# Performance work log

Hardware: AMD Instinct MI355X
Metric: run time of the kernel (lower is better)

The kernel has to match this reference:

```python
import jax, jax.numpy as jnp
import numpy as np

H = 16
NUM_LANDMARKS = 32


def setup_inputs() -> dict:
    key = jax.random.key(0)
    ks = jax.random.split(key, 8)
    B, L, D, hd = 2, 2048, 1024, 64
    x = jax.random.normal(ks[0], (B, L, D), dtype=jnp.float32)
    wscale = 1.0 / np.sqrt(D)
    wq = jax.random.normal(ks[1], (D, D), dtype=jnp.float32) * wscale
    wk = jax.random.normal(ks[2], (D, D), dtype=jnp.float32) * wscale
    wv = jax.random.normal(ks[3], (D, D), dtype=jnp.float32) * wscale
    wo = jax.random.normal(ks[4], (D, D), dtype=jnp.float32) * wscale
    memory_gate = jnp.zeros((1,), dtype=jnp.float32)
    memory_decay = jnp.asarray(2.944, dtype=jnp.float32)
    # standard RoPE angle table: theta_j = 10000^(-2j/hd)
    inv_freq = 1.0 / (10000.0 ** (np.arange(0, hd, 2, dtype=np.float32) / hd))
    ang = np.outer(np.arange(L, dtype=np.float32), inv_freq)  # (L, hd//2)
    freqs_cos = jnp.asarray(np.cos(ang), dtype=jnp.float32)
    freqs_sin = jnp.asarray(np.sin(ang), dtype=jnp.float32)
    # previous-chunk memory: phi features are >= 0, Z accumulates ~NUM_LANDMARKS
    M_old = jax.random.normal(ks[5], (B, H, hd, hd), dtype=jnp.float32) * 0.1
    Z_old = jax.random.uniform(ks[6], (B, H, hd), dtype=jnp.float32) * NUM_LANDMARKS + 1.0
    return {"x": x, "wq": wq, "wk": wk, "wv": wv, "wo": wo,
            "memory_gate": memory_gate, "memory_decay": memory_decay,
            "freqs_cos": freqs_cos, "freqs_sin": freqs_sin,
            "M_old": M_old, "Z_old": Z_old}


def reference(x, wq, wk, wv, wo, memory_gate, memory_decay,
              freqs_cos, freqs_sin, M_old, Z_old):
    B, L, D = x.shape
    hd = D // H

    def proj(w):
        # nn.Linear: x @ W^T, then split heads -> (B, H, L, hd)
        return (x @ w.T).reshape(B, L, H, hd).transpose(0, 2, 1, 3)

    q_base, k_base, v = proj(wq), proj(wk), proj(wv)

    def rope(t):
        # complex multiply on adjacent pairs of the head dim
        tr = t.reshape(B, H, L, hd // 2, 2)
        t0, t1 = tr[..., 0], tr[..., 1]
        cos = freqs_cos[None, None]  # (1,1,L,hd//2)
        sin = freqs_sin[None, None]
        o0 = t0 * cos - t1 * sin
        o1 = t0 * sin + t1 * cos
        return jnp.stack([o0, o1], axis=-1).reshape(B, H, L, hd)

    q_rope, k_rope = rope(q_base), rope(k_base)

    # causal SDPA
    scale = 1.0 / jnp.sqrt(jnp.asarray(hd, dtype=q_rope.dtype))
    scores = jnp.einsum('bhqd,bhkd->bhqk', q_rope, k_rope) * scale
    causal = jnp.tril(jnp.ones((L, L), dtype=bool))
    scores = jnp.where(causal[None, None], scores, jnp.finfo(scores.dtype).min)
    attn = jax.nn.softmax(scores, axis=-1)
    local_out = jnp.einsum('bhqk,bhkd->bhqd', attn, v)

    # linear-attention memory read (uses un-rotated q_base)
    phi_Q = jax.nn.elu(q_base) + 1.0
    num = jnp.einsum('bhld,bhde->bhle', phi_Q, M_old)
    den = jnp.sum(phi_Q * Z_old[:, :, None, :], axis=-1, keepdims=True) + 1e-6
    global_out = num / den
    gate = jax.nn.sigmoid(memory_gate)  # (1,)
    out = local_out + gate * global_out

    # landmark compression: adaptive avg pool == uniform chunk means (L % M == 0)
    def landmarks(t):
        return t.reshape(B, H, NUM_LANDMARKS, L // NUM_LANDMARKS, hd).mean(axis=3)

    phi_K = jax.nn.elu(landmarks(k_base)) + 1.0
    landmark_v = landmarks(v)
    delta_M = jnp.einsum('bhmd,bhme->bhde', phi_K, landmark_v)
    delta_Z = phi_K.sum(axis=-2)

    decay = jax.nn.sigmoid(memory_decay)
    M_new = M_old * decay + delta_M
    Z_new = Z_old * decay + delta_Z

    out = out.transpose(0, 2, 1, 3).reshape(B, L, D)
    y = out @ wo.T
    return y, M_new, Z_new
```

## Files before the change

kernel.cpp:

```cpp
#include <hip/hip_runtime.h>
#include <math.h>

#define NH 16
#define HD 64
#define NB 2
#define LSEQ 2048
#define DM 1024
#define NLM 32

#define OUT_M 4194304
#define OUT_Z 4325376

typedef unsigned short u16;
typedef short bf16x8 __attribute__((ext_vector_type(8)));
typedef float f32x16 __attribute__((ext_vector_type(16)));
typedef unsigned short u16x4 __attribute__((ext_vector_type(4)));
typedef unsigned long long ull;

__device__ __forceinline__ float sigmoidf_(float x) { return 1.0f / (1.0f + __expf(-x)); }
__device__ __forceinline__ float phif_(float x) { return x > 0.0f ? x + 1.0f : __expf(x); }

__device__ __forceinline__ u16 f2b(float f) {
    union { float f; unsigned u; } v; v.f = f;
    unsigned r = v.u + 0x7FFFu + ((v.u >> 16) & 1u);
    return (u16)(r >> 16);
}
__device__ __forceinline__ float b2f(u16 b) {
    union { unsigned u; float f; } v; v.u = ((unsigned)b) << 16; return v.f;
}
__device__ __forceinline__ ull pack4(float a, float b, float c, float d) {
    return (ull)f2b(a) | ((ull)f2b(b) << 16) | ((ull)f2b(c) << 32) | ((ull)f2b(d) << 48);
}
__device__ __forceinline__ int cvtpkbf(float lo, float hi2) {
    int r;
    asm("v_cvt_pk_bf16_f32 %0, %1, %2" : "=v"(r) : "v"(lo), "v"(hi2));
    return r;
}
__device__ __forceinline__ void gload16(const u16* g, u16* l) {
    __builtin_amdgcn_global_load_lds(
        (const __attribute__((address_space(1))) void*)g,
        (__attribute__((address_space(3))) void*)l, 16, 0, 0);
}
__device__ __forceinline__ void block_sync_lds() {
    __builtin_amdgcn_sched_barrier(0);
    asm volatile("s_waitcnt lgkmcnt(0)" ::: "memory");
    __builtin_amdgcn_s_barrier();
    __builtin_amdgcn_sched_barrier(0);
}

__global__ __launch_bounds__(256) void cvt_all(
    const float* __restrict__ x, const float* __restrict__ wq,
    const float* __restrict__ wk, const float* __restrict__ wv,
    const float* __restrict__ wo, u16* __restrict__ dst) {
    size_t i = ((size_t)blockIdx.x * 256 + threadIdx.x) * 8;
    const float* src;
    size_t off;
    if (i < 4194304)      { src = x;  off = i; }
    else if (i < 5242880) { src = wq; off = i - 4194304; }
    else if (i < 6291456) { src = wk; off = i - 5242880; }
    else if (i < 7340032) { src = wv; off = i - 6291456; }
    else                  { src = wo; off = i - 7340032; }
    float4 a = *(const float4*)(src + off);
    float4 b = *(const float4*)(src + off + 4);
    u16 o[8] = {f2b(a.x), f2b(a.y), f2b(a.z), f2b(a.w),
                f2b(b.x), f2b(b.y), f2b(b.z), f2b(b.w)};
    *(int4*)(dst + i) = *(int4*)o;
}

template <int MODE>
__global__ __launch_bounds__(256) void gemm_mfma(
    const u16* __restrict__ A, const u16* __restrict__ W,
    float* __restrict__ Cf, u16* __restrict__ qb, u16* __restrict__ qrp,
    u16* __restrict__ kbp, u16* __restrict__ krp, u16* __restrict__ vbp,
    const float* __restrict__ fcos, const float* __restrict__ fsin) {
    __shared__ u16 As[128 * 64];
    __shared__ u16 Ws[128 * 64];
    const int tid = threadIdx.x;
    const int m0 = blockIdx.x * 128;
    const int n0 = blockIdx.y * 128;
    const int w = tid >> 6;
    const int lane = tid & 63;
    const int l31 = lane & 31;
    const int khalf = lane >> 5;
    const int wr0 = (w >> 1) * 64;
    const int wc0 = (w & 1) * 64;

    const u16* Ag = A + (size_t)m0 * DM;
    const u16* Wg = W + (size_t)n0 * DM;

    const int st_uoff[4] = {w * 4096, w * 4096 + 1024, w * 4096 + 2048, w * 4096 + 3072};
    int st_row[4], st_cc[4];
#pragma unroll
    for (int i = 0; i < 4; ++i) {
        const int off = st_uoff[i] + lane * 16;
        st_row[i] = off >> 7;
        st_cc[i] = ((off >> 4) & 7) ^ (st_row[i] & 7);
    }

    f32x16 acc[2][2];
#pragma unroll
    for (int mf = 0; mf < 2; ++mf)
#pragma unroll
        for (int nf = 0; nf < 2; ++nf)
#pragma unroll
            for (int i = 0; i < 16; ++i) acc[mf][nf][i] = 0.f;

    for (int k0 = 0; k0 < DM; k0 += 64) {
        __syncthreads();
#pragma unroll
        for (int i = 0; i < 4; ++i)
            gload16(Ag + (size_t)st_row[i] * DM + k0 + st_cc[i] * 8,
                    (u16*)((char*)As + st_uoff[i]));
#pragma unroll
        for (int i = 0; i < 4; ++i)
            gload16(Wg + (size_t)st_row[i] * DM + k0 + st_cc[i] * 8,
                    (u16*)((char*)Ws + st_uoff[i]));
        __syncthreads();
#pragma unroll
        for (int ko = 0; ko < 4; ++ko) {
            const int cl = ko * 2 + khalf;
            const int ra0 = wr0 + l31, ra1 = wr0 + 32 + l31;
            const int rb0 = wc0 + l31, rb1 = wc0 + 32 + l31;
            bf16x8 af0 = *(const bf16x8*)((char*)As + ra0 * 128 + ((cl ^ (ra0 & 7)) * 16));
            bf16x8 af1 = *(const bf16x8*)((char*)As + ra1 * 128 + ((cl ^ (ra1 & 7)) * 16));
            bf16x8 bf0 = *(const bf16x8*)((char*)Ws + rb0 * 128 + ((cl ^ (rb0 & 7)) * 16));
            bf16x8 bf1 = *(const bf16x8*)((char*)Ws + rb1 * 128 + ((cl ^ (rb1 & 7)) * 16));
            acc[0][0] = __builtin_amdgcn_mfma_f32_32x32x16_bf16(af0, bf0, acc[0][0], 0, 0, 0);
            acc[0][1] = __builtin_amdgcn_mfma_f32_32x32x16_bf16(af0, bf1, acc[0][1], 0, 0, 0);
            acc[1][0] = __builtin_amdgcn_mfma_f32_32x32x16_bf16(af1, bf0, acc[1][0], 0, 0, 0);
            acc[1][1] = __builtin_amdgcn_mfma_f32_32x32x16_bf16(af1, bf1, acc[1][1], 0, 0, 0);
        }
    }

#pragma unroll
    for (int mf = 0; mf < 2; ++mf) {
#pragma unroll
        for (int nf = 0; nf < 2; ++nf) {
            const int nn = n0 + wc0 + nf * 32 + l31;
#pragma unroll
            for (int reg = 0; reg < 16; ++reg) {
                const int m = m0 + wr0 + mf * 32 + (reg & 3) + 8 * (reg >> 2) + 4 * khalf;
                const float val = acc[mf][nf][reg];
                if (MODE == 1) {
                    Cf[(size_t)m * DM + nn] = val;
                } else {
                    const int b = m >> 11, l = m & (LSEQ - 1);
                    const int mat = nn >> 10;
                    const int n = nn & 1023;
                    const int h = n >> 6, d = n & 63;
                    const size_t hs = (((size_t)(b * NH + h)) * LSEQ + l) * HD + d;
                    const float p = __shfl_xor(val, 1);
                    if (mat == 2) {
                        vbp[hs] = f2b(val);
                    } else {
                        u16* bs = mat ? kbp : qb;
                        u16* rs = mat ? krp : qrp;
                        bs[hs] = f2b(val);
                        const float c = fcos[l * 32 + (d >> 1)];
                        const float s = fsin[l * 32 + (d >> 1)];
                        float o = (d & 1) ? (p * s + val * c) : (val * c - p * s);
                        if (mat == 0) o *= 0.18033688f;
                        rs[hs] = f2b(o);
                    }
                }
            }
        }
    }
}

__global__ __launch_bounds__(256) void landmarks(
    const u16* __restrict__ kbase, const u16* __restrict__ vbase,
    float* __restrict__ lkq, float* __restrict__ lvq) {
    __shared__ float redk[4][HD];
    __shared__ float redv[4][HD];
    const int bh = blockIdx.x >> 5;
    const int m = blockIdx.x & 31;
    const int tid = threadIdx.x;
    const int ls = tid >> 6;
    const int d = tid & 63;
    const u16* kb = kbase + ((size_t)bh * LSEQ + m * 64) * HD;
    const u16* vb = vbase + ((size_t)bh * LSEQ + m * 64) * HD;
    float sk = 0.f, sv = 0.f;
    for (int l = ls; l < 64; l += 4) {
        sk += b2f(kb[(size_t)l * HD + d]);
        sv += b2f(vb[(size_t)l * HD + d]);
    }
    redk[ls][d] = sk;
    redv[ls][d] = sv;
    __syncthreads();
    if (tid < 64) {
        float mk = (redk[0][d] + redk[1][d] + redk[2][d] + redk[3][d]) * (1.0f / 64.0f);
        float mv = (redv[0][d] + redv[1][d] + redv[2][d] + redv[3][d]) * (1.0f / 64.0f);
        lkq[((size_t)bh * NLM + m) * HD + d] = phif_(mk);
        lvq[((size_t)bh * NLM + m) * HD + d] = mv;
    }
}

__global__ __launch_bounds__(256) void mem_update(
    const float* __restrict__ lkq, const float* __restrict__ lvq,
    const float* __restrict__ M_old, const float* __restrict__ Z_old,
    const float* __restrict__ decay_p, float* __restrict__ out) {
    __shared__ float lk[NLM][HD];
    __shared__ float lv[NLM][HD];
    const int bh = blockIdx.x;
    const int tid = threadIdx.x;
    const float decay = sigmoidf_(decay_p[0]);
#pragma unroll
    for (int i = 0; i < 8; ++i) {
        int idx = tid + 256 * i;
        lk[idx >> 6][idx & 63] = lkq[(size_t)bh * (NLM * HD) + idx];
        lv[idx >> 6][idx & 63] = lvq[(size_t)bh * (NLM * HD) + idx];
    }
    __syncthreads();
    const size_t mo = (size_t)bh * HD * HD;
#pragma unroll
    for (int p = 0; p < 16; ++p) {
        int idx = tid + 256 * p;
        int dd = idx >> 6, e = idx & 63;
        float s = 0.f;
#pragma unroll
        for (int m = 0; m < NLM; ++m) s = fmaf(lk[m][dd], lv[m][e], s);
        out[OUT_M + mo + idx] = M_old[mo + idx] * decay + s;
    }
    if (tid < 64) {
        float s = 0.f;
#pragma unroll
        for (int m = 0; m < NLM; ++m) s += lk[m][tid];
        out[OUT_Z + (size_t)bh * HD + tid] = Z_old[(size_t)bh * HD + tid] * decay + s;
    }
}

__global__ __launch_bounds__(256) void combine(
    const u16* __restrict__ qbase, const u16* __restrict__ opart,
    const float2* __restrict__ ml, const float* __restrict__ M_old,
    const float* __restrict__ Z_old, const float* __restrict__ gate_p,
    u16* __restrict__ ctxb) {
    __shared__ float phiQ[64][68];
    __shared__ float Ms[64][64];
    __shared__ float Zs[64];
    const int l0 = blockIdx.x * 64;
    const int bh = blockIdx.y;
    const int b = bh >> 4, h = bh & 15;
    const int tid = threadIdx.x;
    const float gate = sigmoidf_(gate_p[0]);

    {
        const int r = tid >> 2, c0 = (tid & 3) << 4;
        const float* Mo = M_old + (size_t)bh * HD * HD + (size_t)r * HD + c0;
#pragma unroll
        for (int i = 0; i < 4; ++i)
            *reinterpret_cast<float4*>(&Ms[r][c0 + 4 * i]) =
                *reinterpret_cast<const float4*>(Mo + 4 * i);
        if (tid < 64) Zs[tid] = Z_old[(size_t)bh * HD + tid];
        const u16* q = qbase + ((size_t)bh * LSEQ + l0 + r) * HD + c0;
#pragma unroll
        for (int i = 0; i < 4; ++i) {
            u16x4 q4 = *(const u16x4*)(q + 4 * i);
            phiQ[r][c0 + 4 * i + 0] = phif_(b2f(q4[0]));
            phiQ[r][c0 + 4 * i + 1] = phif_(b2f(q4[1]));
            phiQ[r][c0 + 4 * i + 2] = phif_(b2f(q4[2]));
            phiQ[r][c0 + 4 * i + 3] = phif_(b2f(q4[3]));
        }
    }
    __syncthreads();

    const int lr = tid >> 2, sub = tid & 3, e0 = sub << 4;
    float den = 0.f;
#pragma unroll
    for (int i = 0; i < 16; ++i) den = fmaf(phiQ[lr][e0 + i], Zs[e0 + i], den);
    den += __shfl_xor(den, 1);
    den += __shfl_xor(den, 2);
    den += 1e-6f;

    float acc[16] = {};
    for (int dd = 0; dd < 64; ++dd) {
        const float pq = phiQ[lr][dd];
#pragma unroll
        for (int i = 0; i < 16; ++i) acc[i] = fmaf(pq, Ms[dd][e0 + i], acc[i]);
    }
    const float g = gate / den;

    const int row = l0 + lr;
    const float2 m0 = ml[bh * LSEQ + row];
    const float2 m1 = ml[32 * LSEQ + bh * LSEQ + row];
    const float mm = fmaxf(m0.x, m1.x);
    float a0 = exp2f(m0.x - mm) * m0.y;
    float a1 = exp2f(m1.x - mm) * m1.y;
    const float inv = 1.0f / (a0 + a1);
    a0 *= inv; a1 *= inv;

    const size_t prow = ((size_t)bh * LSEQ + row) * HD + e0;
    const u16* o0p = opart + prow;
    const u16* o1p = opart + 4194304 + prow;
    int4 o0a = *(const int4*)o0p;
    int4 o0b = *(const int4*)(o0p + 8);
    int4 o1a = *(const int4*)o1p;
    int4 o1b = *(const int4*)(o1p + 8);
    const u16* u0a = (const u16*)&o0a; const u16* u0b = (const u16*)&o0b;
    const u16* u1a = (const u16*)&o1a; const u16* u1b = (const u16*)&o1b;

    const size_t rowoff = ((size_t)b * LSEQ + row) * DM + h * HD + e0;
    u16 o[16];
#pragma unroll
    for (int i = 0; i < 8; ++i) {
        float att = a0 * b2f(u0a[i]) + a1 * b2f(u1a[i]);
        o[i] = f2b(att + g * acc[i]);
    }
#pragma unroll
    for (int i = 0; i < 8; ++i) {
        float att = a0 * b2f(u0b[i]) + a1 * b2f(u1b[i]);
        o[8 + i] = f2b(att + g * acc[8 + i]);
    }
    *(int4*)(ctxb + rowoff) = *(int4*)o;
    *(int4*)(ctxb + rowoff + 8) = *(int4*)(o + 8);
}

__global__ __launch_bounds__(256) void flash_mfma(
    const u16* __restrict__ qr, const u16* __restrict__ kr,
    const u16* __restrict__ vv, u16* __restrict__ opart,
    float2* __restrict__ ml) {
    __shared__ int4 smem4[2048];
    char* lds = (char*)smem4;

    const int bid = blockIdx.x;
    const int qt = 15 - (bid >> 6);
    const int half = (bid >> 5) & 1;
    const int bh = bid & 31;
    const int q0 = qt * 128;
    const int tid = threadIdx.x;
    const int w = tid >> 6;
    const int lane = tid & 63;
    const int hi = lane >> 5;
    const int l31 = lane & 31;
    const int qw0 = q0 + w * 32;
    const int tdiag = qw0 >> 6;
    const int t0 = half ? (qt + 1) : 0;
    const int t1 = half ? (2 * qt + 2) : (qt + 1);
    const size_t base_bh = (size_t)bh * (LSEQ * HD);

#pragma unroll
    for (int i = 0; i < 4; ++i) {
        int u = tid + 256 * i;
        int row = u >> 3, c = u & 7;
        int4 val = *(const int4*)(qr + base_bh + (size_t)(q0 + row) * HD + c * 8);
        *(int4*)(lds + 16384 + row * 128 + ((c ^ (row & 7)) * 16)) = val;
    }

    int r_[2], c_[2], skoff_[2], svoff_[2];
#pragma unroll
    for (int j = 0; j < 2; ++j) {
        int u = tid + 256 * j;
        int r = u >> 3, cc = u & 7;
        r_[j] = r; c_[j] = cc;
        skoff_[j] = r * 128 + ((cc ^ (r & 7)) * 16);
        int d0 = cc << 3;
        svoff_[j] = (r >> 5) * 4096 + (d0 >> 5) * 2048 + (d0 & 31) * 64
                  + ((((r & 31) >> 3) ^ ((d0 >> 3) & 3)) * 16 + (r & 7) * 2);
    }

    int4 RAk[2], RAv[2], RBk[2], RBv[2];
    auto load_tile = [&](int t, int4* Rk, int4* Rv) {
#pragma unroll
        for (int j = 0; j < 2; ++j) {
            Rk[j] = *(const int4*)(kr + base_bh + (size_t)(t * 64 + r_[j]) * HD + c_[j] * 8);
            Rv[j] = *(const int4*)(vv + base_bh + (size_t)(t * 64 + r_[j]) * HD + c_[j] * 8);
        }
    };
    auto write_tile = [&](int base, int4* Rk, int4* Rv) {
#pragma unroll
        for (int j = 0; j < 2; ++j) {
            *(int4*)(lds + base + skoff_[j]) = Rk[j];
            union { int4 q; u16 h[8]; } uv; uv.q = Rv[j];
            char* vd = lds + base + 8192 + svoff_[j];
#pragma unroll
            for (int e = 0; e < 8; ++e) *(u16*)(vd + e * 64) = uv.h[e];
        }
    };

    load_tile(t0, RAk, RAv);
    block_sync_lds();

    bf16x8 qf[4];
    {
        const char* qp = lds + 16384 + ((w << 5) + l31) * 128;
        const int sw = l31 & 7;
#pragma unroll
        for (int ks = 0; ks < 4; ++ks) {
            int c = 2 * ks + hi;
            qf[ks] = *(const bf16x8*)(qp + ((c ^ sw) * 16));
        }
    }
    write_tile(0, RAk, RAv);
    if (t0 + 1 < t1) load_tile(t0 + 1, RBk, RBv);
    block_sync_lds();

    f32x16 accO[2];
#pragma unroll
    for (int mf = 0; mf < 2; ++mf)
#pragma unroll
        for (int i = 0; i < 16; ++i) accO[mf][i] = 0.f;
    float m_run = -INFINITY, l_run = 0.f;
    const int swK = l31 & 7;
    const int vsw = (l31 >> 3) & 3;

    auto compute_tile = [&](int t, int base) {
        const char* Kb = lds + base;
        const char* Vb = lds + base + 8192;
        f32x16 st0, st1;
#pragma unroll
        for (int i = 0; i < 16; ++i) { st0[i] = 0.f; st1[i] = 0.f; }
        __builtin_amdgcn_s_setprio(1);
#pragma unroll
        for (int ks = 0; ks < 4; ++ks) {
            int cc = 2 * ks + hi;
            bf16x8 kf0 = *(const bf16x8*)(Kb + l31 * 128 + ((cc ^ swK) * 16));
            bf16x8 kf1 = *(const bf16x8*)(Kb + (32 + l31) * 128 + ((cc ^ swK) * 16));
            st0 = __builtin_amdgcn_mfma_f32_32x32x16_bf16(kf0, qf[ks], st0, 0, 0, 0);
            st1 = __builtin_amdgcn_mfma_f32_32x32x16_bf16(kf1, qf[ks], st1, 0, 0, 0);
        }
        __builtin_amdgcn_s_setprio(0);
        bf16x8 va[2][2][2];
#pragma unroll
        for (int sub = 0; sub < 2; ++sub)
#pragma unroll
            for (int kb2 = 0; kb2 < 2; ++kb2)
#pragma unroll
                for (int mf = 0; mf < 2; ++mf)
                    va[sub][kb2][mf] = *(const bf16x8*)(
                        Vb + sub * 4096 + mf * 2048 + l31 * 64 + (((kb2 * 2 + hi) ^ vsw) * 16));

        float s[32];
#pragma unroll
        for (int r = 0; r < 16; ++r) { s[r] = st0[r]; s[16 + r] = st1[r]; }
        if (t == tdiag) {
            const int qg = qw0 + l31;
#pragma unroll
            for (int r = 0; r < 32; ++r) {
                int keyg = t * 64 + (r >> 4) * 32 + (r & 3) + 8 * ((r >> 2) & 3) + 4 * hi;
                if (keyg > qg) s[r] = -INFINITY;
            }
        }
        float t16[16];
#pragma unroll
        for (int r = 0; r < 16; ++r) t16[r] = fmaxf(s[r], s[r + 16]);
        float t8[8];
#pragma unroll
        for (int r = 0; r < 8; ++r) t8[r] = fmaxf(t16[r], t16[r + 8]);
        float t4[4];
#pragma unroll
        for (int r = 0; r < 4; ++r) t4[r] = fmaxf(t8[r], t8[r + 4]);
        float pm = fmaxf(fmaxf(t4[0], t4[1]), fmaxf(t4[2], t4[3]));
        pm = fmaxf(pm, __shfl_xor(pm, 32));
        if (!__all(pm - m_run <= 11.5416f)) {
            const float mn = fmaxf(m_run, pm);
            const float sc = exp2f(m_run - mn);
#pragma unroll
            for (int mf = 0; mf < 2; ++mf)
#pragma unroll
                for (int i = 0; i < 16; ++i) accO[mf][i] *= sc;
            l_run *= sc;
            m_run = mn;
        }
        float p[32];
#pragma unroll
        for (int r = 0; r < 32; ++r) p[r] = exp2f(s[r] - m_run);
        float a16[16];
#pragma unroll
        for (int r = 0; r < 16; ++r) a16[r] = p[r] + p[r + 16];
        float a8[8];
#pragma unroll
        for (int r = 0; r < 8; ++r) a8[r] = a16[r] + a16[r + 8];
        float a4[4];
#pragma unroll
        for (int r = 0; r < 4; ++r) a4[r] = a8[r] + a8[r + 4];
        float ss = (a4[0] + a4[1]) + (a4[2] + a4[3]);
        ss += __shfl_xor(ss, 32);
        l_run += ss;

        int pk[16];
#pragma unroll
        for (int i = 0; i < 16; ++i) pk[i] = cvtpkbf(p[2 * i], p[2 * i + 1]);
        int xp[16];
#pragma unroll
        for (int i = 0; i < 16; ++i) xp[i] = __shfl_xor(pk[i], 32);
        const bool hib = (hi != 0);
        union { int i[4]; bf16x8 v; } pu[4];
#pragma unroll
        for (int g = 0; g < 4; ++g) {
            const int o = g * 4;
            pu[g].i[0] = hib ? xp[o + 2] : pk[o + 0];
            pu[g].i[1] = hib ? xp[o + 3] : pk[o + 1];
            pu[g].i[2] = hib ? pk[o + 2] : xp[o + 0];
            pu[g].i[3] = hib ? pk[o + 3] : xp[o + 1];
        }
        __builtin_amdgcn_s_setprio(1);
        accO[0] = __builtin_amdgcn_mfma_f32_32x32x16_bf16(va[0][0][0], pu[0].v, accO[0], 0, 0, 0);
        accO[1] = __builtin_amdgcn_mfma_f32_32x32x16_bf16(va[0][0][1], pu[0].v, accO[1], 0, 0, 0);
        accO[0] = __builtin_amdgcn_mfma_f32_32x32x16_bf16(va[0][1][0], pu[1].v, accO[0], 0, 0, 0);
        accO[1] = __builtin_amdgcn_mfma_f32_32x32x16_bf16(va[0][1][1], pu[1].v, accO[1], 0, 0, 0);
        accO[0] = __builtin_amdgcn_mfma_f32_32x32x16_bf16(va[1][0][0], pu[2].v, accO[0], 0, 0, 0);
        accO[1] = __builtin_amdgcn_mfma_f32_32x32x16_bf16(va[1][0][1], pu[2].v, accO[1], 0, 0, 0);
        accO[0] = __builtin_amdgcn_mfma_f32_32x32x16_bf16(va[1][1][0], pu[3].v, accO[0], 0, 0, 0);
        accO[1] = __builtin_amdgcn_mfma_f32_32x32x16_bf16(va[1][1][1], pu[3].v, accO[1], 0, 0, 0);
        __builtin_amdgcn_s_setprio(0);
    };

    for (int t = t0; t < t1; t += 2) {
        if (t + 1 < t1) write_tile(16384, RBk, RBv);
        if (t + 2 < t1) load_tile(t + 2, RAk, RAv);
        if (t <= tdiag) compute_tile(t, 0);
        block_sync_lds();
        if (t + 2 < t1) write_tile(0, RAk, RAv);
        if (t + 3 < t1) load_tile(t + 3, RBk, RBv);
        if (t + 1 < t1 && t + 1 <= tdiag) compute_tile(t + 1, 16384);
        block_sync_lds();
    }

    const float invl = (l_run > 0.f) ? (1.0f / l_run) : 0.f;
    const int qg = qw0 + l31;
    u16* obase = opart + (half ? 4194304 : 0) + ((size_t)bh * LSEQ + qg) * HD;
#pragma unroll
    for (int mf = 0; mf < 2; ++mf) {
#pragma unroll
        for (int g = 0; g < 4; ++g) {
            const int d4 = mf * 32 + 8 * g + 4 * hi;
            *(ull*)(obase + d4) = pack4(accO[mf][g * 4 + 0] * invl,
                                        accO[mf][g * 4 + 1] * invl,
                                        accO[mf][g * 4 + 2] * invl,
                                        accO[mf][g * 4 + 3] * invl);
        }
    }
    if (hi == 0)
        ml[(half ? 32 * LSEQ : 0) + bh * LSEQ + qg] = make_float2(m_run, l_run);
}

extern "C" void kernel_launch(void* const* d_in, const int* in_sizes, int n_in,
                              void* d_out, int out_size, void* d_ws, size_t ws_size,
                              hipStream_t stream) {
    const float* x     = (const float*)d_in[0];
    const float* wq    = (const float*)d_in[1];
    const float* wk    = (const float*)d_in[2];
    const float* wv    = (const float*)d_in[3];
    const float* wo    = (const float*)d_in[4];
    const float* gate  = (const float*)d_in[5];
    const float* decay = (const float*)d_in[6];
    const float* fcos  = (const float*)d_in[7];
    const float* fsin  = (const float*)d_in[8];
    const float* M_old = (const float*)d_in[9];
    const float* Z_old = (const float*)d_in[10];
    float* out = (float*)d_out;

    u16* xb     = (u16*)d_ws;
    u16* wqkv   = xb + 4194304;
    u16* wob    = wqkv + 3145728;
    u16* q_rope = wob + 1048576;
    u16* q_base = q_rope + 4194304;
    u16* k_rope = q_base + 4194304;
    u16* k_base = k_rope + 4194304;
    u16* v      = k_base + 4194304;
    u16* opart  = v + 4194304;
    float* wsf  = (float*)wqkv;
    float* lkq  = wsf;
    float* lvq  = wsf + 65536;
    float2* ml  = (float2*)(wsf + 131072);
    u16* ctxb   = xb;

    dim3 bb(256);
    cvt_all<<<dim3(4096), bb, 0, stream>>>(x, wq, wk, wv, wo, xb);

    gemm_mfma<4><<<dim3(32, 24), bb, 0, stream>>>(xb, wqkv, nullptr, q_base, q_rope,
                                                  k_base, k_rope, v, fcos, fsin);

    landmarks<<<dim3(NB * NH * NLM), bb, 0, stream>>>(k_base, v, lkq, lvq);
    mem_update<<<dim3(NB * NH), bb, 0, stream>>>(lkq, lvq, M_old, Z_old, decay, out);
    flash_mfma<<<dim3(1024), bb, 0, stream>>>(q_rope, k_rope, v, opart, ml);
    combine<<<dim3(LSEQ / 64, NB * NH), bb, 0, stream>>>(q_base, opart, ml, M_old,
                                                         Z_old, gate, ctxb);

    gemm_mfma<1><<<dim3(32, 8), bb, 0, stream>>>(ctxb, wob, out, nullptr, nullptr,
                                                 nullptr, nullptr, nullptr, nullptr, nullptr);
}
```

Before: 173.2 us.

## Pre-swizzle Q/K/V tiles in GEMM epilogue and stage via direct global-to-LDS loads

```diff
diff --git a/kernel.cpp b/kernel.cpp
--- a/kernel.cpp
+++ b/kernel.cpp
@@ -41,7 +41,13 @@
         (const __attribute__((address_space(1))) void*)g,
         (__attribute__((address_space(3))) void*)l, 16, 0, 0);
 }
-__device__ __forceinline__ void block_sync_lds() {
+__device__ __forceinline__ void sync_vm0() {
+    __builtin_amdgcn_sched_barrier(0);
+    asm volatile("s_waitcnt vmcnt(0)" ::: "memory");
+    __builtin_amdgcn_s_barrier();
+    __builtin_amdgcn_sched_barrier(0);
+}
+__device__ __forceinline__ void sync_lgkm0() {
     __builtin_amdgcn_sched_barrier(0);
     asm volatile("s_waitcnt lgkmcnt(0)" ::: "memory");
     __builtin_amdgcn_s_barrier();
@@ -70,8 +76,8 @@
 template <int MODE>
 __global__ __launch_bounds__(256) void gemm_mfma(
     const u16* __restrict__ A, const u16* __restrict__ W,
-    float* __restrict__ Cf, u16* __restrict__ qb, u16* __restrict__ qrp,
-    u16* __restrict__ kbp, u16* __restrict__ krp, u16* __restrict__ vbp,
+    float* __restrict__ Cf, u16* __restrict__ qb, u16* __restrict__ qt_,
+    u16* __restrict__ kbp, u16* __restrict__ kt, u16* __restrict__ vt,
     const float* __restrict__ fcos, const float* __restrict__ fsin) {
     __shared__ u16 As[128 * 64];
     __shared__ u16 Ws[128 * 64];
@@ -148,19 +154,30 @@
                     const int mat = nn >> 10;
                     const int n = nn & 1023;
                     const int h = n >> 6, d = n & 63;
-                    const size_t hs = (((size_t)(b * NH + h)) * LSEQ + l) * HD + d;
+                    const int bh = b * NH + h;
+                    const size_t hs = (((size_t)bh) * LSEQ + l) * HD + d;
                     const float p = __shfl_xor(val, 1);
                     if (mat == 2) {
-                        vbp[hs] = f2b(val);
+                        const int t = l >> 6, r = l & 63;
+                        vt[((size_t)(bh * 32 + t)) * 4096 + (r >> 5) * 2048 +
+                           (d >> 5) * 1024 + (d & 31) * 32 +
+                           ((((r & 31) >> 3) ^ ((d >> 3) & 3)) * 8) + (r & 7)] = f2b(val);
                     } else {
-                        u16* bs = mat ? kbp : qb;
-                        u16* rs = mat ? krp : qrp;
-                        bs[hs] = f2b(val);
                         const float c = fcos[l * 32 + (d >> 1)];
                         const float s = fsin[l * 32 + (d >> 1)];
                         float o = (d & 1) ? (p * s + val * c) : (val * c - p * s);
-                        if (mat == 0) o *= 0.18033688f;
-                        rs[hs] = f2b(o);
+                        if (mat == 0) {
+                            o *= 0.18033688f;
+                            qb[hs] = f2b(val);
+                            const int qtile = l >> 7, row = l & 127;
+                            qt_[((size_t)(bh * 16 + qtile)) * 8192 + row * 64 +
+                                (((d >> 3) ^ (row & 7)) * 8) + (d & 7)] = f2b(o);
+                        } else {
+                            kbp[hs] = f2b(val);
+                            const int t = l >> 6, r = l & 63;
+                            kt[((size_t)(bh * 32 + t)) * 4096 + r * 64 +
+                               (((d >> 3) ^ (r & 7)) * 8) + (d & 7)] = f2b(o);
+                        }
                     }
                 }
             }
@@ -169,30 +186,42 @@
 }
 
 __global__ __launch_bounds__(256) void landmarks(
-    const u16* __restrict__ kbase, const u16* __restrict__ vbase,
+    const u16* __restrict__ kbase, const u16* __restrict__ vt,
     float* __restrict__ lkq, float* __restrict__ lvq) {
     __shared__ float redk[4][HD];
-    __shared__ float redv[4][HD];
+    __shared__ float redv[8][HD];
     const int bh = blockIdx.x >> 5;
     const int m = blockIdx.x & 31;
     const int tid = threadIdx.x;
     const int ls = tid >> 6;
     const int d = tid & 63;
     const u16* kb = kbase + ((size_t)bh * LSEQ + m * 64) * HD;
-    const u16* vb = vbase + ((size_t)bh * LSEQ + m * 64) * HD;
-    float sk = 0.f, sv = 0.f;
-    for (int l = ls; l < 64; l += 4) {
-        sk += b2f(kb[(size_t)l * HD + d]);
-        sv += b2f(vb[(size_t)l * HD + d]);
-    }
+    float sk = 0.f;
+    for (int l = ls; l < 64; l += 4) sk += b2f(kb[(size_t)l * HD + d]);
     redk[ls][d] = sk;
-    redv[ls][d] = sv;
+
+    const u16* vtile = vt + ((size_t)(bh * 32 + m)) * 4096;
+#pragma unroll
+    for (int j = 0; j < 2; ++j) {
+        const int slot = tid + 256 * j;
+        const int kg = slot >> 6, dd = slot & 63;
+        const u16* p = vtile + (kg >> 2) * 2048 + (dd >> 5) * 1024 + (dd & 31) * 32 +
+                       (((kg & 3) ^ ((dd >> 3) & 3)) * 8);
+        int4 raw = *(const int4*)p;
+        const u16* u = (const u16*)&raw;
+        float s = 0.f;
+#pragma unroll
+        for (int e = 0; e < 8; ++e) s += b2f(u[e]);
+        redv[kg][dd] = s;
+    }
     __syncthreads();
     if (tid < 64) {
         float mk = (redk[0][d] + redk[1][d] + redk[2][d] + redk[3][d]) * (1.0f / 64.0f);
-        float mv = (redv[0][d] + redv[1][d] + redv[2][d] + redv[3][d]) * (1.0f / 64.0f);
+        float sv = 0.f;
+#pragma unroll
+        for (int kg = 0; kg < 8; ++kg) sv += redv[kg][d];
         lkq[((size_t)bh * NLM + m) * HD + d] = phif_(mk);
-        lvq[((size_t)bh * NLM + m) * HD + d] = mv;
+        lvq[((size_t)bh * NLM + m) * HD + d] = sv * (1.0f / 64.0f);
     }
 }
 
@@ -316,8 +345,8 @@
 }
 
 __global__ __launch_bounds__(256) void flash_mfma(
-    const u16* __restrict__ qr, const u16* __restrict__ kr,
-    const u16* __restrict__ vv, u16* __restrict__ opart,
+    const u16* __restrict__ qt_, const u16* __restrict__ kt,
+    const u16* __restrict__ vt, u16* __restrict__ opart,
     float2* __restrict__ ml) {
     __shared__ int4 smem4[2048];
     char* lds = (char*)smem4;
@@ -326,59 +355,34 @@
     const int qt = 15 - (bid >> 6);
     const int half = (bid >> 5) & 1;
     const int bh = bid & 31;
-    const int q0 = qt * 128;
     const int tid = threadIdx.x;
     const int w = tid >> 6;
     const int lane = tid & 63;
     const int hi = lane >> 5;
     const int l31 = lane & 31;
-    const int qw0 = q0 + w * 32;
+    const int qw0 = qt * 128 + w * 32;
     const int tdiag = qw0 >> 6;
     const int t0 = half ? (qt + 1) : 0;
     const int t1 = half ? (2 * qt + 2) : (qt + 1);
-    const size_t base_bh = (size_t)bh * (LSEQ * HD);
-
-#pragma unroll
-    for (int i = 0; i < 4; ++i) {
-        int u = tid + 256 * i;
-        int row = u >> 3, c = u & 7;
-        int4 val = *(const int4*)(qr + base_bh + (size_t)(q0 + row) * HD + c * 8);
-        *(int4*)(lds + 16384 + row * 128 + ((c ^ (row & 7)) * 16)) = val;
-    }
-
-    int r_[2], c_[2], skoff_[2], svoff_[2];
-#pragma unroll
-    for (int j = 0; j < 2; ++j) {
-        int u = tid + 256 * j;
-        int r = u >> 3, cc = u & 7;
-        r_[j] = r; c_[j] = cc;
-        skoff_[j] = r * 128 + ((cc ^ (r & 7)) * 16);
-        int d0 = cc << 3;
-        svoff_[j] = (r >> 5) * 4096 + (d0 >> 5) * 2048 + (d0 & 31) * 64
-                  + ((((r & 31) >> 3) ^ ((d0 >> 3) & 3)) * 16 + (r & 7) * 2);
-    }
-
-    int4 RAk[2], RAv[2], RBk[2], RBv[2];
-    auto load_tile = [&](int t, int4* Rk, int4* Rv) {
+
+    auto stage_tile = [&](int t, int base) {
+        const u16* ks = kt + ((size_t)(bh * 32 + t)) * 4096;
+        const u16* vs = vt + ((size_t)(bh * 32 + t)) * 4096;
 #pragma unroll
         for (int j = 0; j < 2; ++j) {
-            Rk[j] = *(const int4*)(kr + base_bh + (size_t)(t * 64 + r_[j]) * HD + c_[j] * 8);
-            Rv[j] = *(const int4*)(vv + base_bh + (size_t)(t * 64 + r_[j]) * HD + c_[j] * 8);
+            gload16(ks + tid * 8 + j * 2048, (u16*)(lds + base + w * 1024 + j * 4096));
+            gload16(vs + tid * 8 + j * 2048, (u16*)(lds + base + 8192 + w * 1024 + j * 4096));
         }
     };
-    auto write_tile = [&](int base, int4* Rk, int4* Rv) {
-#pragma unroll
-        for (int j = 0; j < 2; ++j) {
-            *(int4*)(lds + base + skoff_[j]) = Rk[j];
-            union { int4 q; u16 h[8]; } uv; uv.q = Rv[j];
-            char* vd = lds + base + 8192 + svoff_[j];
-#pragma unroll
-            for (int e = 0; e < 8; ++e) *(u16*)(vd + e * 64) = uv.h[e];
-        }
-    };
-
-    load_tile(t0, RAk, RAv);
-    block_sync_lds();
+
+    {
+        const u16* qs = qt_ + ((size_t)(bh * 16 + qt)) * 8192;
+#pragma unroll
+        for (int i = 0; i < 4; ++i)
+            gload16(qs + tid * 8 + i * 2048, (u16*)(lds + 16384 + w * 1024 + i * 4096));
+    }
+    stage_tile(t0, 0);
+    sync_vm0();
 
     bf16x8 qf[4];
     {
@@ -390,9 +394,7 @@
             qf[ks] = *(const bf16x8*)(qp + ((c ^ sw) * 16));
         }
     }
-    write_tile(0, RAk, RAv);
-    if (t0 + 1 < t1) load_tile(t0 + 1, RBk, RBv);
-    block_sync_lds();
+    sync_lgkm0();
 
     f32x16 accO[2];
 #pragma unroll
@@ -505,15 +507,12 @@
         __builtin_amdgcn_s_setprio(0);
     };
 
-    for (int t = t0; t < t1; t += 2) {
-        if (t + 1 < t1) write_tile(16384, RBk, RBv);
-        if (t + 2 < t1) load_tile(t + 2, RAk, RAv);
-        if (t <= tdiag) compute_tile(t, 0);
-        block_sync_lds();
-        if (t + 2 < t1) write_tile(0, RAk, RAv);
-        if (t + 3 < t1) load_tile(t + 3, RBk, RBv);
-        if (t + 1 < t1 && t + 1 <= tdiag) compute_tile(t + 1, 16384);
-        block_sync_lds();
+    int curb = 0;
+    for (int t = t0; t < t1; ++t) {
+        if (t + 1 < t1) stage_tile(t + 1, (curb ^ 1) * 16384);
+        if (t <= tdiag) compute_tile(t, curb * 16384);
+        sync_vm0();
+        curb ^= 1;
     }
 
     const float invl = (l_run > 0.f) ? (1.0f / l_run) : 0.f;
@@ -553,12 +552,12 @@
     u16* xb     = (u16*)d_ws;
     u16* wqkv   = xb + 4194304;
     u16* wob    = wqkv + 3145728;
-    u16* q_rope = wob + 1048576;
-    u16* q_base = q_rope + 4194304;
-    u16* k_rope = q_base + 4194304;
-    u16* k_base = k_rope + 4194304;
-    u16* v      = k_base + 4194304;
-    u16* opart  = v + 4194304;
+    u16* qt_    = wob + 1048576;
+    u16* q_base = qt_ + 4194304;
+    u16* kt     = q_base + 4194304;
+    u16* k_base = kt + 4194304;
+    u16* vt     = k_base + 4194304;
+    u16* opart  = vt + 4194304;
     float* wsf  = (float*)wqkv;
     float* lkq  = wsf;
     float* lvq  = wsf + 65536;
@@ -568,12 +567,12 @@
     dim3 bb(256);
     cvt_all<<<dim3(4096), bb, 0, stream>>>(x, wq, wk, wv, wo, xb);
 
-    gemm_mfma<4><<<dim3(32, 24), bb, 0, stream>>>(xb, wqkv, nullptr, q_base, q_rope,
-                                                  k_base, k_rope, v, fcos, fsin);
-
-    landmarks<<<dim3(NB * NH * NLM), bb, 0, stream>>>(k_base, v, lkq, lvq);
+    gemm_mfma<4><<<dim3(32, 24), bb, 0, stream>>>(xb, wqkv, nullptr, q_base, qt_,
+                                                  k_base, kt, vt, fcos, fsin);
+
+    landmarks<<<dim3(NB * NH * NLM), bb, 0, stream>>>(k_base, vt, lkq, lvq);
     mem_update<<<dim3(NB * NH), bb, 0, stream>>>(lkq, lvq, M_old, Z_old, decay, out);
-    flash_mfma<<<dim3(1024), bb, 0, stream>>>(q_rope, k_rope, v, opart, ml);
+    flash_mfma<<<dim3(1024), bb, 0, stream>>>(qt_, kt, vt, opart, ml);
     combine<<<dim3(LSEQ / 64, NB * NH), bb, 0, stream>>>(q_base, opart, ml, M_old,
                                                          Z_old, gate, ctxb);
 
```

Measured after the change: 192.0 us. 1.11x slower.
